# Kernel optimization log

Measured on AMD Instinct MI355X. Metric: run time of the kernel, lower is better.

## Reference

```python
import jax, jax.numpy as jnp
import numpy as np

NBINS = 30  # matches init kwarg `bins`


def setup_inputs() -> dict:
    key = jax.random.key(0)
    k1, k2, k3, k4 = jax.random.split(key, 4)
    B, C, Q, D = 128, 4, 32, 2048
    # cosine-similarity matrix in [-1, 1): required so bin indices land in [0, NBINS)
    simmat = jax.random.uniform(k1, (B, C, Q, D), jnp.float32, minval=-1.0, maxval=1.0)
    dlens = jax.random.randint(k2, (B,), 1, D, dtype=jnp.int32)
    # token ids; -1 marks padding (masked out of the histogram weights)
    dtoks = jax.random.randint(k3, (B, D), -1, 100, dtype=jnp.int32)
    qtoks = jax.random.randint(k4, (B, Q), -1, 100, dtype=jnp.int32)
    return {"simmat": simmat, "dlens": dlens, "dtoks": dtoks, "qtoks": qtoks}


def reference(simmat, dlens, dtoks, qtoks):
    B, C, Q, D = simmat.shape
    # bin index per similarity value; torch's .int() truncates toward zero,
    # which equals astype(int32) here since all values are non-negative.
    bins = ((simmat + 1.00001) / 2.0 * (NBINS - 1)).astype(jnp.int32)  # [B,C,Q,D]
    # padding mask: count a (q,d) pair only if both tokens are valid
    w = ((dtoks != -1)[:, None, :] & (qtoks != -1)[:, :, None]).astype(jnp.float32)  # [B,Q,D]
    w4 = jnp.broadcast_to(w[:, None, :, :], (B, C, Q, D))
    # weighted bincount per (b,c,q) row via one flat scatter-add
    rows = jnp.arange(B * C * Q, dtype=jnp.int32)[:, None]            # [BCQ,1]
    flat_idx = (rows * NBINS + bins.reshape(B * C * Q, D)).reshape(-1)
    hist = jnp.zeros((B * C * Q * NBINS,), jnp.float32).at[flat_idx].add(w4.reshape(-1))
    return hist.reshape(B, C, Q, NBINS)
```

## Files before the change

kernel.cpp:

```cpp
#include <hip/hip_runtime.h>


#define NBINS 30
#define DIM   2048
#define QDIM  32
#define CDIM  4

__global__ __launch_bounds__(256) void CountHistogram_kernel(
    const float* __restrict__ simmat,
    const int*   __restrict__ dtoks,
    const int*   __restrict__ qtoks,
    float*       __restrict__ out)
{
    const int bid  = blockIdx.x;
    const int q    = bid & (QDIM - 1);
    const int b    = bid / (CDIM * QDIM);
    const int tid  = threadIdx.x;
    const int wave = tid >> 6;

    __shared__ int h[4][32];
    if (tid < 128) ((int*)h)[tid] = 0;

    const int qt = qtoks[b * QDIM + q];
    __syncthreads();

    if (qt != -1) {
        const float4* sm = (const float4*)(simmat + (size_t)bid * DIM);
        const int4*   dt = (const int4*)(dtoks  + (size_t)b   * DIM);
        #pragma unroll
        for (int ch = 0; ch < 2; ++ch) {
            const int idx = ch * 256 + tid;
            const float4 s = sm[idx];
            const int4   t = dt[idx];
            int b0 = (int)((s.x + 1.00001f) / 2.0f * 29.0f);
            int b1 = (int)((s.y + 1.00001f) / 2.0f * 29.0f);
            int b2 = (int)((s.z + 1.00001f) / 2.0f * 29.0f);
            int b3 = (int)((s.w + 1.00001f) / 2.0f * 29.0f);
            if (t.x != -1) atomicAdd(&h[wave][b0], 1);
            if (t.y != -1) atomicAdd(&h[wave][b1], 1);
            if (t.z != -1) atomicAdd(&h[wave][b2], 1);
            if (t.w != -1) atomicAdd(&h[wave][b3], 1);
        }
    }
    __syncthreads();

    if (tid < NBINS) {
        out[(size_t)bid * NBINS + tid] =
            (float)(h[0][tid] + h[1][tid] + h[2][tid] + h[3][tid]);
    }
}

extern "C" void kernel_launch(void* const* d_in, const int* in_sizes, int n_in,
                              void* d_out, int out_size, void* d_ws, size_t ws_size,
                              hipStream_t stream) {
    const float* simmat = (const float*)d_in[0];
    const int*   dtoks  = (const int*)d_in[2];
    const int*   qtoks  = (const int*)d_in[3];
    float*       out    = (float*)d_out;

    const int nrows = 128 * CDIM * QDIM;
    CountHistogram_kernel<<<nrows, 256, 0, stream>>>(simmat, dtoks, qtoks, out);
}
```

Baseline: 29.80 us.

## Precompute doc-token validity bitmasks and process one histogram row per wavefront

```diff
diff --git a/kernel.cpp b/kernel.cpp
--- a/kernel.cpp
+++ b/kernel.cpp
@@ -5,48 +5,63 @@
 #define DIM   2048
 #define QDIM  32
 #define CDIM  4
+#define BDIM  128
+
+__global__ __launch_bounds__(64) void make_mask_kernel(
+    const int* __restrict__ dtoks, unsigned int* __restrict__ masks)
+{
+    const int b    = blockIdx.x;
+    const int lane = threadIdx.x;
+    #pragma unroll
+    for (int w = 0; w < 32; ++w) {
+        const int t = dtoks[b * DIM + w * 64 + lane];
+        const unsigned long long m = __ballot(t != -1);
+        if (lane == 0) {
+            masks[b * 64 + 2 * w]     = (unsigned int)(m & 0xffffffffu);
+            masks[b * 64 + 2 * w + 1] = (unsigned int)(m >> 32);
+        }
+    }
+}
 
 __global__ __launch_bounds__(256) void CountHistogram_kernel(
-    const float* __restrict__ simmat,
-    const int*   __restrict__ dtoks,
-    const int*   __restrict__ qtoks,
-    float*       __restrict__ out)
+    const float*        __restrict__ simmat,
+    const unsigned int* __restrict__ masks,
+    const int*          __restrict__ qtoks,
+    float*              __restrict__ out)
 {
-    const int bid  = blockIdx.x;
-    const int q    = bid & (QDIM - 1);
-    const int b    = bid / (CDIM * QDIM);
     const int tid  = threadIdx.x;
     const int wave = tid >> 6;
+    const int lane = tid & 63;
+    const int row  = blockIdx.x * 4 + wave;
+    const int q    = row & (QDIM - 1);
+    const int b    = row >> 7;
 
     __shared__ int h[4][32];
-    if (tid < 128) ((int*)h)[tid] = 0;
+    if (lane < 32) h[wave][lane] = 0;
 
     const int qt = qtoks[b * QDIM + q];
-    __syncthreads();
 
     if (qt != -1) {
-        const float4* sm = (const float4*)(simmat + (size_t)bid * DIM);
-        const int4*   dt = (const int4*)(dtoks  + (size_t)b   * DIM);
+        const float4* sm = (const float4*)(simmat + (size_t)row * DIM);
+        const unsigned int* mk = masks + b * 64;
         #pragma unroll
-        for (int ch = 0; ch < 2; ++ch) {
-            const int idx = ch * 256 + tid;
-            const float4 s = sm[idx];
-            const int4   t = dt[idx];
+        for (int j = 0; j < 8; ++j) {
+            const float4 s = sm[j * 64 + lane];
+            const unsigned int mw  = mk[j * 8 + (lane >> 3)];
+            const unsigned int nib = (mw >> (4 * (lane & 7))) & 0xF;
             int b0 = (int)((s.x + 1.00001f) / 2.0f * 29.0f);
             int b1 = (int)((s.y + 1.00001f) / 2.0f * 29.0f);
             int b2 = (int)((s.z + 1.00001f) / 2.0f * 29.0f);
             int b3 = (int)((s.w + 1.00001f) / 2.0f * 29.0f);
-            if (t.x != -1) atomicAdd(&h[wave][b0], 1);
-            if (t.y != -1) atomicAdd(&h[wave][b1], 1);
-            if (t.z != -1) atomicAdd(&h[wave][b2], 1);
-            if (t.w != -1) atomicAdd(&h[wave][b3], 1);
+            if (nib & 1u) atomicAdd(&h[wave][b0], 1);
+            if (nib & 2u) atomicAdd(&h[wave][b1], 1);
+            if (nib & 4u) atomicAdd(&h[wave][b2], 1);
+            if (nib & 8u) atomicAdd(&h[wave][b3], 1);
         }
     }
-    __syncthreads();
 
-    if (tid < NBINS) {
-        out[(size_t)bid * NBINS + tid] =
-            (float)(h[0][tid] + h[1][tid] + h[2][tid] + h[3][tid]);
+    if (lane < NBINS) {
+        out[(size_t)row * NBINS + lane] = (float)h[wave][lane];
     }
 }
 
@@ -57,7 +72,10 @@
     const int*   dtoks  = (const int*)d_in[2];
     const int*   qtoks  = (const int*)d_in[3];
     float*       out    = (float*)d_out;
+    unsigned int* masks = (unsigned int*)d_ws;
 
-    const int nrows = 128 * CDIM * QDIM;
-    CountHistogram_kernel<<<nrows, 256, 0, stream>>>(simmat, dtoks, qtoks, out);
+    make_mask_kernel<<<BDIM, 64, 0, stream>>>(dtoks, masks);
+
+    const int nrows = BDIM * CDIM * QDIM;
+    CountHistogram_kernel<<<nrows / 4, 256, 0, stream>>>(simmat, masks, qtoks, out);
 }
```

Result: slower. 35.99 us (+20.8%).

## Map one histogram row per wave with rotated per-group LDS sub-histograms

Applied to the files above, without the earlier changes.

```diff
diff --git a/kernel.cpp b/kernel.cpp
--- a/kernel.cpp
+++ b/kernel.cpp
@@ -5,6 +5,7 @@
 #define DIM   2048
 #define QDIM  32
 #define CDIM  4
+#define BDIM  128
 
 __global__ __launch_bounds__(256) void CountHistogram_kernel(
     const float* __restrict__ simmat,
@@ -12,41 +13,46 @@
     const int*   __restrict__ qtoks,
     float*       __restrict__ out)
 {
-    const int bid  = blockIdx.x;
-    const int q    = bid & (QDIM - 1);
-    const int b    = bid / (CDIM * QDIM);
     const int tid  = threadIdx.x;
     const int wave = tid >> 6;
+    const int lane = tid & 63;
+    const int row  = blockIdx.x * 4 + wave;
+    const int q    = row & (QDIM - 1);
+    const int b    = row >> 7;
 
-    __shared__ int h[4][32];
-    if (tid < 128) ((int*)h)[tid] = 0;
+    __shared__ int hs[4][4][32];
+    int* hw = &hs[wave][0][0];
+    hw[lane]      = 0;
+    hw[lane + 64] = 0;
 
-    const int qt = qtoks[b * QDIM + q];
-    __syncthreads();
+    const int qt   = qtoks[b * QDIM + q];
+    const int rotg = (lane & 48) >> 1;
+    int* hg = &hs[wave][lane >> 4][0];
 
     if (qt != -1) {
-        const float4* sm = (const float4*)(simmat + (size_t)bid * DIM);
+        const float4* sm = (const float4*)(simmat + (size_t)row * DIM);
         const int4*   dt = (const int4*)(dtoks  + (size_t)b   * DIM);
         #pragma unroll
-        for (int ch = 0; ch < 2; ++ch) {
-            const int idx = ch * 256 + tid;
-            const float4 s = sm[idx];
-            const int4   t = dt[idx];
+        for (int j = 0; j < 8; ++j) {
+            const float4 s = sm[j * 64 + lane];
+            const int4   t = dt[j * 64 + lane];
             int b0 = (int)((s.x + 1.00001f) / 2.0f * 29.0f);
             int b1 = (int)((s.y + 1.00001f) / 2.0f * 29.0f);
             int b2 = (int)((s.z + 1.00001f) / 2.0f * 29.0f);
             int b3 = (int)((s.w + 1.00001f) / 2.0f * 29.0f);
-            if (t.x != -1) atomicAdd(&h[wave][b0], 1);
-            if (t.y != -1) atomicAdd(&h[wave][b1], 1);
-            if (t.z != -1) atomicAdd(&h[wave][b2], 1);
-            if (t.w != -1) atomicAdd(&h[wave][b3], 1);
+            if (t.x != -1) atomicAdd(&hg[(b0 + rotg) & 31], 1);
+            if (t.y != -1) atomicAdd(&hg[(b1 + rotg) & 31], 1);
+            if (t.z != -1) atomicAdd(&hg[(b2 + rotg) & 31], 1);
+            if (t.w != -1) atomicAdd(&hg[(b3 + rotg) & 31], 1);
         }
     }
-    __syncthreads();
 
-    if (tid < NBINS) {
-        out[(size_t)bid * NBINS + tid] =
-            (float)(h[0][tid] + h[1][tid] + h[2][tid] + h[3][tid]);
+    if (lane < NBINS) {
+        int sum = 0;
+        #pragma unroll
+        for (int g = 0; g < 4; ++g)
+            sum += hs[wave][g][(lane + 8 * g) & 31];
+        out[(size_t)row * NBINS + lane] = (float)sum;
     }
 }
 
@@ -58,6 +64,6 @@
     const int*   qtoks  = (const int*)d_in[3];
     float*       out    = (float*)d_out;
 
-    const int nrows = 128 * CDIM * QDIM;
-    CountHistogram_kernel<<<nrows, 256, 0, stream>>>(simmat, dtoks, qtoks, out);
+    const int nrows = BDIM * CDIM * QDIM;
+    CountHistogram_kernel<<<nrows / 4, 256, 0, stream>>>(simmat, dtoks, qtoks, out);
 }
```

Result: faster. 28.28 us (-5.1%).
